# Optimization experiments

Hardware: AMD Instinct MI355X
Metric: run time of the kernel (lower is better)

Reference implementation:

```python
import jax, jax.numpy as jnp
import numpy as np

B, S, D, R, H = 4, 2048, 1024, 256, 8
NI, NP, NO, K = 8, 32, 8, 3
DH = R // H


def _householder_chain(x, vs):
    # x: [B,S,R], vs: [B,S,K,R]; apply K Householder reflections sequentially
    def step(carry, v):
        vn = v * jax.lax.rsqrt(jnp.sum(v * v, axis=-1, keepdims=True) + 1e-8)
        vTx = jnp.sum(carry * vn, axis=-1, keepdims=True)
        return carry - 2.0 * vn * vTx, None
    out, _ = jax.lax.scan(step, x, jnp.moveaxis(vs, 2, 0))
    return out


def _circuit_down(x, in_neurons, proc_neurons, input_weights, proc_idx):
    # soft mixture of input-neuron projections: d_model -> rank
    all_proj = jnp.einsum('bsd,ndr->bsnr', x, in_neurons)
    xr = jnp.einsum('bsnr,bsn->bsr', all_proj, input_weights)
    return _householder_chain(xr, proc_neurons[proc_idx])


def setup_inputs():
    key = jax.random.key(0)
    ks = jax.random.split(key, 14)
    n = lambda k, shape, sc: jax.random.normal(k, shape, jnp.float32) * sc
    inv_d, inv_r = 1.0 / np.sqrt(D), 1.0 / np.sqrt(R)
    return {
        'x': n(ks[0], (B, S, D), 1.0),
        'q_in': n(ks[1], (NI, D, R), inv_d),
        'q_proc': n(ks[2], (NP, R), inv_r),
        'k_in': n(ks[3], (NI, D, R), inv_d),
        'k_proc': n(ks[4], (NP, R), inv_r),
        'v_in': n(ks[5], (NI, D, R), inv_d),
        'v_proc': n(ks[6], (NP, R), inv_r),
        'o_proc': n(ks[7], (NP, R), inv_r),
        'o_out': n(ks[8], (NO, R, D), inv_r),
        'rd_in': n(ks[9], (NI, D), inv_d),
        'rd_proc': n(ks[10], (NP, D), inv_d),
        'ru_out': n(ks[11], (NO, R), inv_r),
        'ru_proc': n(ks[12], (NP, R), inv_r),
    }


def reference(x, q_in, q_proc, k_in, k_proc, v_in, v_proc, o_proc, o_out,
              rd_in, rd_proc, ru_out, ru_proc):
    # --- router (down): soft input weights + top-k process indices ---
    input_weights = jax.nn.softmax(x @ rd_in.T, axis=-1)          # [B,S,NI]
    _, pidx = jax.lax.top_k(x @ rd_proc.T, K)                     # [B,S,K]

    q = _circuit_down(x, q_in, q_proc, input_weights, pidx)      # [B,S,R]
    k = _circuit_down(x, k_in, k_proc, input_weights, pidx)
    v = _circuit_down(x, v_in, v_proc, input_weights, pidx)

    qh = q.reshape(B, S, H, DH)
    kh = k.reshape(B, S, H, DH)
    vh = v.reshape(B, S, H, DH)
    scores = jnp.einsum('bqhd,bkhd->bhqk', qh, kh) / np.sqrt(DH)
    attn = jax.nn.softmax(scores, axis=-1)
    o = jnp.einsum('bhqk,bkhd->bqhd', attn, vh).reshape(B, S, R)  # [B,S,R]

    # --- router (up): soft output weights + top-k process indices ---
    output_weights = jax.nn.softmax(o @ ru_out.T, axis=-1)        # [B,S,NO]
    _, pidx_u = jax.lax.top_k(o @ ru_proc.T, K)                   # [B,S,K]

    oh = _householder_chain(o, o_proc[pidx_u])                    # [B,S,R]
    out = jnp.einsum('bsr,bsn,nrd->bsd', oh, output_weights, o_out)
    return out
```

## Files before the change

### kernel.cpp

```cpp
#include <hip/hip_runtime.h>
#include <math.h>

#define NI 8
#define NP 32
#define TOPK 3

typedef _Float16 f16;
typedef f16 f16x8 __attribute__((ext_vector_type(8)));
typedef f16 f16x4 __attribute__((ext_vector_type(4)));
typedef float f32x4 __attribute__((ext_vector_type(4)));

__device__ __forceinline__ float wave_sum(float v) {
  #pragma unroll
  for (int off = 32; off; off >>= 1) v += __shfl_xor(v, off);
  return v;
}

__device__ __forceinline__ void gload16(const void* g, void* l) {
  __builtin_amdgcn_global_load_lds(
      (const __attribute__((address_space(1))) unsigned int*)g,
      (__attribute__((address_space(3))) unsigned int*)l, 16, 0, 0);
}

__device__ __forceinline__ unsigned int pack_f16x2(float x) {
  f16 h = (f16)x;
  f16 l = (f16)(x - (float)h);
  return (unsigned int)__builtin_bit_cast(unsigned short, h)
       | ((unsigned int)__builtin_bit_cast(unsigned short, l) << 16);
}

__device__ __forceinline__ void unpack8(const unsigned int* p, f16x8& hi, f16x8& lo) {
  uint4 w0 = *reinterpret_cast<const uint4*>(p);
  uint4 w1 = *reinterpret_cast<const uint4*>(p + 4);
  union { unsigned int u[4]; f16x8 v; } H, L;
  H.u[0] = (w0.x & 0xffffu) | (w0.y << 16);
  L.u[0] = (w0.x >> 16)     | (w0.y & 0xffff0000u);
  H.u[1] = (w0.z & 0xffffu) | (w0.w << 16);
  L.u[1] = (w0.z >> 16)     | (w0.w & 0xffff0000u);
  H.u[2] = (w1.x & 0xffffu) | (w1.y << 16);
  L.u[2] = (w1.x >> 16)     | (w1.y & 0xffff0000u);
  H.u[3] = (w1.z & 0xffffu) | (w1.w << 16);
  L.u[3] = (w1.z >> 16)     | (w1.w & 0xffff0000u);
  hi = H.v; lo = L.v;
}

template<int CHUNKS>
__global__ __launch_bounds__(256) void router_kernel(
    const float* __restrict__ X,
    const float* __restrict__ Wsm,
    const float* __restrict__ Wtk,
    float* __restrict__ iw, int* __restrict__ pidx)
{
  const int tid = threadIdx.x, wave = tid >> 6, lane = tid & 63;
  const int t = blockIdx.x * 4 + wave;
  __shared__ float sc[4][40];
  const int Kin = CHUNKS * 256;
  const float4* Xp = reinterpret_cast<const float4*>(X + (size_t)t * Kin);
  float4 xv[CHUNKS];
  #pragma unroll
  for (int c = 0; c < CHUNKS; ++c) xv[c] = Xp[c * 64 + lane];

  for (int w = 0; w < 40; ++w) {
    const float* Wr = (w < NI) ? (Wsm + (size_t)w * Kin) : (Wtk + (size_t)(w - NI) * Kin);
    const float4* Wp = reinterpret_cast<const float4*>(Wr);
    float p = 0.f;
    #pragma unroll
    for (int c = 0; c < CHUNKS; ++c) {
      float4 wv = Wp[c * 64 + lane];
      p = fmaf(xv[c].x, wv.x, p); p = fmaf(xv[c].y, wv.y, p);
      p = fmaf(xv[c].z, wv.z, p); p = fmaf(xv[c].w, wv.w, p);
    }
    p = wave_sum(p);
    if (lane == 0) sc[wave][w] = p;
  }
  float s = (lane < NI) ? sc[wave][lane] : -3.0e38f;
  float m = s;
  #pragma unroll
  for (int off = 4; off; off >>= 1) m = fmaxf(m, __shfl_xor(m, off));
  float e = expf(s - m);
  float sum = e;
  #pragma unroll
  for (int off = 4; off; off >>= 1) sum += __shfl_xor(sum, off);
  if (lane < NI) iw[(size_t)t * NI + lane] = e / sum;

  float v = (lane < NP) ? sc[wave][NI + lane] : -3.0e38f;
  int idx = lane;
  #pragma unroll
  for (int j = 0; j < TOPK; ++j) {
    float bv = v; int bi = idx;
    #pragma unroll
    for (int off = 32; off; off >>= 1) {
      float ov = __shfl_xor(bv, off); int oi = __shfl_xor(bi, off);
      if (ov > bv || (ov == bv && oi < bi)) { bv = ov; bi = oi; }
    }
    if (lane == 0) pidx[t * TOPK + j] = bi;
    if (idx == bi) v = -3.0e38f;
  }
}

__global__ __launch_bounds__(256) void pack_bt(
    const float* __restrict__ S, f16* __restrict__ Dh, f16* __restrict__ Dl,
    int C, int K)
{
  __shared__ float T[64][65];
  const int tid = threadIdx.x;
  const int kb = blockIdx.x * 64, cb = blockIdx.y * 64;
  const int tr = tid >> 4, tc = (tid & 15) * 4;
  #pragma unroll
  for (int i = 0; i < 4; ++i) {
    float4 v = *reinterpret_cast<const float4*>(&S[(size_t)(kb + tr + i * 16) * C + cb + tc]);
    T[tr + i * 16][tc + 0] = v.x; T[tr + i * 16][tc + 1] = v.y;
    T[tr + i * 16][tc + 2] = v.z; T[tr + i * 16][tc + 3] = v.w;
  }
  __syncthreads();
  #pragma unroll
  for (int i = 0; i < 4; ++i) {
    int c = tr + i * 16;
    f16x4 vh, vl;
    #pragma unroll
    for (int q = 0; q < 4; ++q) {
      float a = T[tc + q][c];
      f16 h = (f16)a;
      vh[q] = h;
      vl[q] = (f16)(a - (float)h);
    }
    *reinterpret_cast<f16x4*>(&Dh[(size_t)(cb + c) * K + kb + tc]) = vh;
    *reinterpret_cast<f16x4*>(&Dl[(size_t)(cb + c) * K + kb + tc]) = vl;
  }
}

__global__ __launch_bounds__(256) void pack_split(
    const float* __restrict__ S, f16* __restrict__ Dh, f16* __restrict__ Dl,
    size_t n8)
{
  size_t i = ((size_t)blockIdx.x * 256 + threadIdx.x);
  if (i >= n8) return;
  const float* s = S + i * 8;
  float4 a = *reinterpret_cast<const float4*>(s);
  float4 b = *reinterpret_cast<const float4*>(s + 4);
  float v[8] = {a.x, a.y, a.z, a.w, b.x, b.y, b.z, b.w};
  f16x8 h, l;
  #pragma unroll
  for (int j = 0; j < 8; ++j) {
    f16 hh = (f16)v[j];
    h[j] = hh;
    l[j] = (f16)(v[j] - (float)hh);
  }
  *reinterpret_cast<f16x8*>(Dh + i * 8) = h;
  *reinterpret_cast<f16x8*>(Dl + i * 8) = l;
}

#define TBM 128
#define TBN 128
#define TBK 32

__global__ __launch_bounds__(256, 2) void gemm_split2(
    const f16* __restrict__ Xh, const f16* __restrict__ Xl, int Kin,
    const float* __restrict__ W,
    const f16* __restrict__ Bth, const f16* __restrict__ Btl,
    float* __restrict__ C, int ldC, int Ktot)
{
  __shared__ f16x8 AhL[512];
  __shared__ f16x8 AlL[512];
  __shared__ f16x8 BhL[512];
  __shared__ f16x8 BlL[512];
  __shared__ float Ws[TBM][NI];

  const int tid = threadIdx.x;
  const int wave = tid >> 6, lane = tid & 63;
  const int wm = wave >> 1, wn = wave & 1;
  const int fr = lane & 15, ks = lane >> 4;
  const int row0 = blockIdx.x * TBM, c0 = blockIdx.y * TBN;

  for (int i = tid; i < TBM * NI; i += 256)
    Ws[i >> 3][i & 7] = W[(size_t)(row0 + (i >> 3)) * NI + (i & 7)];

  const int s1 = 256 + tid;
  const int ar0 = tid >> 2, kg0 = ((tid & 3) - (ar0 >> 1)) & 3;
  const int ar1 = s1 >> 2,  kg1 = ((s1 & 3) - (ar1 >> 1)) & 3;

  const f16* xh0 = Xh + (size_t)(row0 + ar0) * Kin + kg0 * 8;
  const f16* xh1 = Xh + (size_t)(row0 + ar1) * Kin + kg1 * 8;
  const f16* xl0 = Xl + (size_t)(row0 + ar0) * Kin + kg0 * 8;
  const f16* xl1 = Xl + (size_t)(row0 + ar1) * Kin + kg1 * 8;
  const f16* bh0 = Bth + (size_t)(c0 + ar0) * Ktot + kg0 * 8;
  const f16* bh1 = Bth + (size_t)(c0 + ar1) * Ktot + kg1 * 8;
  const f16* bl0 = Btl + (size_t)(c0 + ar0) * Ktot + kg0 * 8;
  const f16* bl1 = Btl + (size_t)(c0 + ar1) * Ktot + kg1 * 8;

  f16x8* AhW = &AhL[wave * 64];
  f16x8* AlW = &AlL[wave * 64];
  f16x8* BhW = &BhL[wave * 64];
  f16x8* BlW = &BlL[wave * 64];

  f32x4 acc[4][4] = {};
  f32x4 cac[4][4] = {};

  int n = 0, dk0 = 0;
  for (int kt = 0; kt < Ktot; kt += TBK) {
    __syncthreads();
    gload16(xh0 + dk0, AhW);
    gload16(xh1 + dk0, AhW + 256);
    gload16(xl0 + dk0, AlW);
    gload16(xl1 + dk0, AlW + 256);
    gload16(bh0 + kt, BhW);
    gload16(bh1 + kt, BhW + 256);
    gload16(bl0 + kt, BlW);
    gload16(bl1 + kt, BlW + 256);
    __syncthreads();

    f16x8 ah[4], al[4], bh[4], bl[4];
    #pragma unroll
    for (int mf = 0; mf < 4; ++mf) {
      int ar = wm * 64 + mf * 16 + fr;
      int sl = ar * 4 + (((ar >> 1) + ks) & 3);
      ah[mf] = AhL[sl]; al[mf] = AlL[sl];
    }
    #pragma unroll
    for (int nf = 0; nf < 4; ++nf) {
      int bc = wn * 64 + nf * 16 + fr;
      int sl = bc * 4 + (((bc >> 1) + ks) & 3);
      bh[nf] = BhL[sl]; bl[nf] = BlL[sl];
// ... 17 lines not shown
        float w2 = Ws[wm * 64 + mf * 16 + ks * 4 + 2][n];
        float w3 = Ws[wm * 64 + mf * 16 + ks * 4 + 3][n];
        #pragma unroll
        for (int nf = 0; nf < 4; ++nf) {
          cac[mf][nf][0] = fmaf(w0, acc[mf][nf][0], cac[mf][nf][0]);
          cac[mf][nf][1] = fmaf(w1, acc[mf][nf][1], cac[mf][nf][1]);
          cac[mf][nf][2] = fmaf(w2, acc[mf][nf][2], cac[mf][nf][2]);
          cac[mf][nf][3] = fmaf(w3, acc[mf][nf][3], cac[mf][nf][3]);
          acc[mf][nf] = (f32x4){0.f, 0.f, 0.f, 0.f};
        }
      }
      ++n;
    }
  }

  #pragma unroll
  for (int mf = 0; mf < 4; ++mf)
    #pragma unroll
    for (int nf = 0; nf < 4; ++nf) {
      int col = c0 + wn * 64 + nf * 16 + fr;
      #pragma unroll
      for (int j = 0; j < 4; ++j) {
        int row = row0 + wm * 64 + mf * 16 + ks * 4 + j;
        C[(size_t)row * ldC + col] = cac[mf][nf][j];
      }
    }
}

#define SBM 128
#define SBN 64
#define SBK 32

__global__ __launch_bounds__(256, 3) void gemm_split(
    const float* __restrict__ X, int Kin,
    const float* __restrict__ W,
    const f16* __restrict__ Bth, const f16* __restrict__ Btl,
    float* __restrict__ C, int ldC, int Ktot)
{
  __shared__ f16x8 AhU[SBM * 4];
  __shared__ f16x8 AlU[SBM * 4];
  __shared__ f16x8 BhU[SBN * 4];
  __shared__ f16x8 BlU[SBN * 4];
  __shared__ float Ws[SBM][NI];

  const int tid = threadIdx.x;
  const int row0 = blockIdx.x * SBM;
  const int c0 = blockIdx.y * SBN;

  const int wave = tid >> 6, lane = tid & 63;
  const int wm = wave >> 1, wn = wave & 1;
  const int fr = lane & 15, ks = lane >> 4;

  for (int i = tid; i < SBM * NI; i += 256)
    Ws[i >> 3][i & 7] = W[(size_t)(row0 + (i >> 3)) * NI + (i & 7)];

  const int arow = tid >> 1, ahalf = tid & 1;
  const float* xrow = X + (size_t)(row0 + arow) * Kin + ahalf * 16;
  const int bcol = tid >> 2;
  const int bks = (tid & 3) ^ (bcol & 3);
  const f16* bsh = Bth + (size_t)(c0 + bcol) * Ktot + bks * 8;
  const f16* bsl = Btl + (size_t)(c0 + bcol) * Ktot + bks * 8;

  f32x4 acc[4][2] = {};

  int n = 0, dk0 = 0;
  for (int kt = 0; kt < Ktot; kt += SBK) {
    __syncthreads();
    {
      float4 v0 = *reinterpret_cast<const float4*>(xrow + dk0);
      float4 v1 = *reinterpret_cast<const float4*>(xrow + dk0 + 4);
      float4 v2 = *reinterpret_cast<const float4*>(xrow + dk0 + 8);
      float4 v3 = *reinterpret_cast<const float4*>(xrow + dk0 + 12);
      float wgt = Ws[arow][n];
      float a[16] = {v0.x, v0.y, v0.z, v0.w, v1.x, v1.y, v1.z, v1.w,
                     v2.x, v2.y, v2.z, v2.w, v3.x, v3.y, v3.z, v3.w};
      f16x8 h0, h1, l0, l1;
      #pragma unroll
      for (int j = 0; j < 8; ++j) {
        float p0 = a[j] * wgt, p1 = a[8 + j] * wgt;
        f16 hh0 = (f16)p0, hh1 = (f16)p1;
        h0[j] = hh0; l0[j] = (f16)(p0 - (float)hh0);
        h1[j] = hh1; l1[j] = (f16)(p1 - (float)hh1);
      }
      const int sw = arow & 3;
      AhU[arow * 4 + ((ahalf * 2 + 0) ^ sw)] = h0;
      AhU[arow * 4 + ((ahalf * 2 + 1) ^ sw)] = h1;
      AlU[arow * 4 + ((ahalf * 2 + 0) ^ sw)] = l0;
      AlU[arow * 4 + ((ahalf * 2 + 1) ^ sw)] = l1;
      BhU[tid] = *reinterpret_cast<const f16x8*>(bsh + kt);
      BlU[tid] = *reinterpret_cast<const f16x8*>(bsl + kt);
    }
    __syncthreads();
    f16x8 ah[4], al[4], bh[2], bl[2];
    #pragma unroll
    for (int mf = 0; mf < 4; ++mf) {
      int ar = wm * 64 + mf * 16 + fr;
      int s = ar * 4 + (ks ^ (ar & 3));
      ah[mf] = AhU[s]; al[mf] = AlU[s];
    }
    #pragma unroll
    for (int nf = 0; nf < 2; ++nf) {
      int bc = wn * 32 + nf * 16 + fr;
      int s = bc * 4 + (ks ^ (bc & 3));
      bh[nf] = BhU[s]; bl[nf] = BlU[s];
    }
    #pragma unroll
    for (int mf = 0; mf < 4; ++mf)
      #pragma unroll
      for (int nf = 0; nf < 2; ++nf) {
        acc[mf][nf] = __builtin_amdgcn_mfma_f32_16x16x32_f16(ah[mf], bh[nf], acc[mf][nf], 0, 0, 0);
        acc[mf][nf] = __builtin_amdgcn_mfma_f32_16x16x32_f16(ah[mf], bl[nf], acc[mf][nf], 0, 0, 0);
        acc[mf][nf] = __builtin_amdgcn_mfma_f32_16x16x32_f16(al[mf], bh[nf], acc[mf][nf], 0, 0, 0);
      }
    dk0 += SBK;
    if (dk0 == Kin) { dk0 = 0; ++n; }
  }
  #pragma unroll
  for (int mf = 0; mf < 4; ++mf)
    #pragma unroll
    for (int nf = 0; nf < 2; ++nf) {
      int col = c0 + wn * 32 + nf * 16 + fr;
      #pragma unroll
      for (int j = 0; j < 4; ++j) {
        int row = row0 + wm * 64 + mf * 16 + ks * 4 + j;
        C[(size_t)row * ldC + col] = acc[mf][nf][j];
      }
    }
}

#define GBM 128
#define GBN 128
#define GBK 16
#define GBMp 132

__global__ __launch_bounds__(256) void gemm_mix(
    const float* __restrict__ X, int Kin,
    const float* __restrict__ W,
    const float* __restrict__ Bm0, const float* __restrict__ Bm1, const float* __restrict__ Bm2,
    int ldB, float* __restrict__ C, int ldC, int Nz)
{
  __shared__ float As[GBK][GBMp];
  __shared__ float Bs[GBK][GBMp];
  __shared__ float Ws[GBM][NI];
  const int tid = threadIdx.x;
  const int row0 = blockIdx.x * GBM;
  const int z = blockIdx.z;
  const float* Bm = (z == 0) ? Bm0 : (z == 1) ? Bm1 : Bm2;
  const int c0 = blockIdx.y * GBN;
// ... 40 lines not shown
      #pragma unroll
      for (int i = 0; i < 8; ++i)
        #pragma unroll
        for (int j = 0; j < 8; ++j)
          acc[i][j] = fmaf(av[i], bv[j], acc[i][j]);
    }
    dk0 += GBK;
    if (dk0 == Kin) { dk0 = 0; ++n; }
  }
  #pragma unroll
  for (int i = 0; i < 8; ++i) {
    int row = row0 + tr * 8 + i;
    float* Cp = C + (size_t)row * ldC + z * Nz + c0 + tc * 8;
    float4 o0 = {acc[i][0], acc[i][1], acc[i][2], acc[i][3]};
    float4 o1 = {acc[i][4], acc[i][5], acc[i][6], acc[i][7]};
    *reinterpret_cast<float4*>(Cp) = o0;
    *reinterpret_cast<float4*>(Cp + 4) = o1;
  }
}

__global__ __launch_bounds__(256) void hh_kernel(
    float* __restrict__ X, int ldX,
    const float* __restrict__ P0, const float* __restrict__ P1, const float* __restrict__ P2,
    const int* __restrict__ pidx)
{
  const int tid = threadIdx.x, wave = tid >> 6, lane = tid & 63;
  const int t = blockIdx.x * 4 + wave;
  const int circ = blockIdx.y;
  const float* P = (circ == 0) ? P0 : (circ == 1) ? P1 : P2;
  float* xp = X + (size_t)t * ldX + circ * 256;
  float4 x4 = *reinterpret_cast<float4*>(xp + lane * 4);
  #pragma unroll
  for (int j = 0; j < TOPK; ++j) {
    int id = pidx[t * TOPK + j];
    const float* vp = P + (size_t)id * 256;
    float4 v4 = *reinterpret_cast<const float4*>(vp + lane * 4);
    float ss = v4.x * v4.x + v4.y * v4.y + v4.z * v4.z + v4.w * v4.w;
    ss = wave_sum(ss);
    float inv = 1.0f / sqrtf(ss + 1e-8f);
    float4 vn = {v4.x * inv, v4.y * inv, v4.z * inv, v4.w * inv};
    float dt = vn.x * x4.x + vn.y * x4.y + vn.z * x4.z + vn.w * x4.w;
    dt = wave_sum(dt);
    float d2 = 2.0f * dt;
    x4.x = fmaf(-d2, vn.x, x4.x);
    x4.y = fmaf(-d2, vn.y, x4.y);
    x4.z = fmaf(-d2, vn.z, x4.z);
    x4.w = fmaf(-d2, vn.w, x4.w);
  }
  *reinterpret_cast<float4*>(xp + lane * 4) = x4;
}

__global__ __launch_bounds__(256, 2) void attn_mfma(
    const float* __restrict__ qkv, float* __restrict__ O)
{
  __shared__ f16 Kh[64][40];
  __shared__ f16 Kl[64][40];
  __shared__ unsigned int Vtp[32][68];
  __shared__ unsigned int Pp[4][32][68];

  const int tid = threadIdx.x, wave = tid >> 6, lane = tid & 63;
  const int c = lane & 15, g = lane >> 4;
  const int bh = blockIdx.y, b = bh >> 3, h = bh & 7;
  const int q0 = blockIdx.x * 128;
  const size_t tbase = (size_t)b * 2048;
  const float SCALE = 0.17677669529663687f;

  f16x8 qh[2], ql[2];
  #pragma unroll
  for (int qt = 0; qt < 2; ++qt) {
    const int row = q0 + wave * 32 + qt * 16 + c;
    const float* qp = qkv + (tbase + row) * 768 + h * 32 + g * 8;
    float4 a = *reinterpret_cast<const float4*>(qp);
    float4 b4 = *reinterpret_cast<const float4*>(qp + 4);
    float qv[8] = {a.x, a.y, a.z, a.w, b4.x, b4.y, b4.z, b4.w};
    #pragma unroll
    for (int j = 0; j < 8; ++j) {
      float xs = qv[j] * SCALE;
      f16 hh = (f16)xs;
      qh[qt][j] = hh;
      ql[qt][j] = (f16)(xs - (float)hh);
    }
  }

  f32x4 sacc[2][4];
  f32x4 oacc[2][2] = {};
  float mrow[2][4] = {{-INFINITY, -INFINITY, -INFINITY, -INFINITY},
                      {-INFINITY, -INFINITY, -INFINITY, -INFINITY}};
  float lrow[2][4] = {};

  for (int k0 = 0; k0 < 2048; k0 += 64) {
    __syncthreads();
    {
      const int kj = tid >> 2, dq = (tid & 3) * 8;
      const float* kp = qkv + (tbase + k0 + kj) * 768 + 256 + h * 32 + dq;
      float4 ka = *reinterpret_cast<const float4*>(kp);
      float4 kb = *reinterpret_cast<const float4*>(kp + 4);
      float kv[8] = {ka.x, ka.y, ka.z, ka.w, kb.x, kb.y, kb.z, kb.w};
      f16x8 khi, klo;
      #pragma unroll
      for (int j = 0; j < 8; ++j) {
        f16 hh = (f16)kv[j];
        khi[j] = hh;
        klo[j] = (f16)(kv[j] - (float)hh);
      }
      *reinterpret_cast<f16x8*>(&Kh[kj][dq]) = khi;
      *reinterpret_cast<f16x8*>(&Kl[kj][dq]) = klo;

      const int vk = tid & 63, vq = (tid >> 6) * 8;
      const float* vp = qkv + (tbase + k0 + vk) * 768 + 512 + h * 32 + vq;
      float4 va = *reinterpret_cast<const float4*>(vp);
      float4 vb = *reinterpret_cast<const float4*>(vp + 4);
      float vv[8] = {va.x, va.y, va.z, va.w, vb.x, vb.y, vb.z, vb.w};
      #pragma unroll
      for (int j = 0; j < 8; ++j) Vtp[vq + j][vk] = pack_f16x2(vv[j]);
    }
    __syncthreads();

    #pragma unroll
    for (int s = 0; s < 4; ++s) {
      f16x8 kbh = *reinterpret_cast<const f16x8*>(&Kh[s * 16 + c][g * 8]);
      f16x8 kbl = *reinterpret_cast<const f16x8*>(&Kl[s * 16 + c][g * 8]);
      #pragma unroll
      for (int qt = 0; qt < 2; ++qt) {
        f32x4 acc = {0.f, 0.f, 0.f, 0.f};
        acc = __builtin_amdgcn_mfma_f32_16x16x32_f16(qh[qt], kbh, acc, 0, 0, 0);
        acc = __builtin_amdgcn_mfma_f32_16x16x32_f16(qh[qt], kbl, acc, 0, 0, 0);
        acc = __builtin_amdgcn_mfma_f32_16x16x32_f16(ql[qt], kbh, acc, 0, 0, 0);
        sacc[qt][s] = acc;
      }
    }

    float alpha[2][4];
    #pragma unroll
    for (int qt = 0; qt < 2; ++qt)
      #pragma unroll
      for (int r = 0; r < 4; ++r) {
        float mt = fmaxf(fmaxf(sacc[qt][0][r], sacc[qt][1][r]),
// ... 1 lines not shown
        #pragma unroll
        for (int off = 1; off < 16; off <<= 1) mt = fmaxf(mt, __shfl_xor(mt, off));
        float mn = fmaxf(mrow[qt][r], mt);
        float al = __expf(mrow[qt][r] - mn);
        mrow[qt][r] = mn;
        alpha[qt][r] = al;
        float ps = 0.f;
        #pragma unroll
        for (int s = 0; s < 4; ++s) {
          float p = __expf(sacc[qt][s][r] - mn);
          sacc[qt][s][r] = p;
          ps += p;
        }
        #pragma unroll
        for (int off = 1; off < 16; off <<= 1) ps += __shfl_xor(ps, off);
        lrow[qt][r] = lrow[qt][r] * al + ps;
      }

    #pragma unroll
    for (int qt = 0; qt < 2; ++qt)
      #pragma unroll
      for (int s = 0; s < 4; ++s)
        #pragma unroll
        for (int r = 0; r < 4; ++r)
          Pp[wave][qt * 16 + g * 4 + r][s * 16 + c] = pack_f16x2(sacc[qt][s][r]);

    #pragma unroll
    for (int qt = 0; qt < 2; ++qt)
      #pragma unroll
      for (int dh = 0; dh < 2; ++dh)
        #pragma unroll
        for (int r = 0; r < 4; ++r) oacc[qt][dh][r] *= alpha[qt][r];

    #pragma unroll
    for (int ch = 0; ch < 2; ++ch) {
      f16x8 pah[2], pal[2];
      #pragma unroll
      for (int qt = 0; qt < 2; ++qt)
        unpack8(&Pp[wave][qt * 16 + c][ch * 32 + g * 8], pah[qt], pal[qt]);
      #pragma unroll
      for (int dh = 0; dh < 2; ++dh) {
        f16x8 vh, vl;
        unpack8(&Vtp[dh * 16 + c][ch * 32 + g * 8], vh, vl);
        #pragma unroll
        for (int qt = 0; qt < 2; ++qt) {
          oacc[qt][dh] = __builtin_amdgcn_mfma_f32_16x16x32_f16(pah[qt], vh, oacc[qt][dh], 0, 0, 0);
          oacc[qt][dh] = __builtin_amdgcn_mfma_f32_16x16x32_f16(pah[qt], vl, oacc[qt][dh], 0, 0, 0);
          oacc[qt][dh] = __builtin_amdgcn_mfma_f32_16x16x32_f16(pal[qt], vh, oacc[qt][dh], 0, 0, 0);
        }
      }
    }
  }

  #pragma unroll
  for (int qt = 0; qt < 2; ++qt)
    #pragma unroll
    for (int r = 0; r < 4; ++r) {
      float inv = 1.0f / lrow[qt][r];
      int row = q0 + wave * 32 + qt * 16 + g * 4 + r;
      #pragma unroll
      for (int dh = 0; dh < 2; ++dh)
        O[(tbase + row) * 256 + h * 32 + dh * 16 + c] = oacc[qt][dh][r] * inv;
    }
}

__global__ __launch_bounds__(256) void attn_kernel(
// ... 79 lines not shown
  oacc /= lf;
  O[(tbase + q0 + wave * 2 + r) * 256 + h * 32 + d] = oacc;
}

extern "C" void kernel_launch(void* const* d_in, const int* in_sizes, int n_in,
                              void* d_out, int out_size, void* d_ws, size_t ws_size,
                              hipStream_t stream) {
  const float* x       = (const float*)d_in[0];
  const float* q_in    = (const float*)d_in[1];
  const float* q_proc  = (const float*)d_in[2];
  const float* k_in    = (const float*)d_in[3];
  const float* k_proc  = (const float*)d_in[4];
  const float* v_in    = (const float*)d_in[5];
  const float* v_proc  = (const float*)d_in[6];
  const float* o_proc  = (const float*)d_in[7];
  const float* o_out   = (const float*)d_in[8];
  const float* rd_in   = (const float*)d_in[9];
  const float* rd_proc = (const float*)d_in[10];
  const float* ru_out  = (const float*)d_in[11];
  const float* ru_proc = (const float*)d_in[12];
  float* out = (float*)d_out;
  float* qkv = (float*)d_out;

  const size_t NEED  = (768ull << 10) + 768ull * 8192 * 2 * 2;
  const size_t NEED2 = (768ull << 10) + 768ull * 8192 * 2 * 2
                     + 8192ull * 1024 * 2 * 2;

  if (ws_size >= NEED2) {
    char* wsb = (char*)d_ws;
    float* iw    = (float*)wsb;
    float* owt   = (float*)(wsb + (256 << 10));
    int*   pidx  = (int*)(wsb + (512 << 10));
    int*   pidxu = (int*)(wsb + (640 << 10));
    char*  R1    = wsb + (768 << 10);
    f16* bth_q = (f16*)R1;
    f16* btl_q = (f16*)(R1 + 768ull * 8192 * 2);
    char*  R2    = R1 + 768ull * 8192 * 2 * 2;
    f16* Xh = (f16*)R2;
    f16* Xl = (f16*)(R2 + 8192ull * 1024 * 2);
    float* obuf = (float*)R2;
    f16* Oh    = (f16*)(R2 + (8192ull * 256 * 4));
    f16* Ol    = (f16*)(R2 + (8192ull * 256 * 4) + 8192ull * 256 * 2);
    f16* bth_o = (f16*)(R2 + (8192ull * 256 * 4) + 8192ull * 256 * 2 * 2);
    f16* btl_o = (f16*)(R2 + (8192ull * 256 * 4) + 8192ull * 256 * 2 * 2 + 2048ull * 1024 * 2);

    router_kernel<4><<<dim3(2048), dim3(256), 0, stream>>>(x, rd_in, rd_proc, iw, pidx);
    pack_split<<<dim3(4096), dim3(256), 0, stream>>>(x, Xh, Xl, 8192ull * 1024 / 8);
    pack_bt<<<dim3(128, 4), dim3(256), 0, stream>>>(q_in, bth_q,                 btl_q,                 256, 8192);
    pack_bt<<<dim3(128, 4), dim3(256), 0, stream>>>(k_in, bth_q + 256ull * 8192, btl_q + 256ull * 8192, 256, 8192);
    pack_bt<<<dim3(128, 4), dim3(256), 0, stream>>>(v_in, bth_q + 512ull * 8192, btl_q + 512ull * 8192, 256, 8192);
    gemm_split2<<<dim3(64, 6), dim3(256), 0, stream>>>(Xh, Xl, 1024, iw, bth_q, btl_q, qkv, 768, 8192);
    hh_kernel<<<dim3(2048, 3), dim3(256), 0, stream>>>(qkv, 768, q_proc, k_proc, v_proc, pidx);
    pack_bt<<<dim3(32, 16), dim3(256), 0, stream>>>(o_out, bth_o, btl_o, 1024, 2048);
    attn_mfma<<<dim3(16, 32), dim3(256), 0, stream>>>(qkv, obuf);
    router_kernel<1><<<dim3(2048), dim3(256), 0, stream>>>(obuf, ru_out, ru_proc, owt, pidxu);
    hh_kernel<<<dim3(2048, 1), dim3(256), 0, stream>>>(obuf, 256, o_proc, o_proc, o_proc, pidxu);
    pack_split<<<dim3(1024), dim3(256), 0, stream>>>(obuf, Oh, Ol, 8192ull * 256 / 8);
    gemm_split2<<<dim3(64, 8), dim3(256), 0, stream>>>(Oh, Ol, 256, owt, bth_o, btl_o, out, 1024, 2048);
  } else if (ws_size >= NEED) {
    char* wsb = (char*)d_ws;
    float* iw    = (float*)wsb;
    float* owt   = (float*)(wsb + (256 << 10));
    int*   pidx  = (int*)(wsb + (512 << 10));
    int*   pidxu = (int*)(wsb + (640 << 10));
    char*  Xr    = wsb + (768 << 10);
    f16* bth_q = (f16*)Xr;
    f16* btl_q = (f16*)(Xr + 768ull * 8192 * 2);
    float* obuf = (float*)Xr;
    f16* bth_o = (f16*)(Xr + (8ull << 20));
    f16* btl_o = (f16*)(Xr + (8ull << 20) + 1024ull * 2048 * 2);

    router_kernel<4><<<dim3(2048), dim3(256), 0, stream>>>(x, rd_in, rd_proc, iw, pidx);
    pack_bt<<<dim3(128, 4), dim3(256), 0, stream>>>(q_in, bth_q,                 btl_q,                 256, 8192);
    pack_bt<<<dim3(128, 4), dim3(256), 0, stream>>>(k_in, bth_q + 256ull * 8192, btl_q + 256ull * 8192, 256, 8192);
    pack_bt<<<dim3(128, 4), dim3(256), 0, stream>>>(v_in, bth_q + 512ull * 8192, btl_q + 512ull * 8192, 256, 8192);
    gemm_split<<<dim3(64, 12), dim3(256), 0, stream>>>(x, 1024, iw, bth_q, btl_q, qkv, 768, 8192);
    hh_kernel<<<dim3(2048, 3), dim3(256), 0, stream>>>(qkv, 768, q_proc, k_proc, v_proc, pidx);
    pack_bt<<<dim3(32, 16), dim3(256), 0, stream>>>(o_out, bth_o, btl_o, 1024, 2048);
    attn_mfma<<<dim3(16, 32), dim3(256), 0, stream>>>(qkv, obuf);
    router_kernel<1><<<dim3(2048), dim3(256), 0, stream>>>(obuf, ru_out, ru_proc, owt, pidxu);
    hh_kernel<<<dim3(2048, 1), dim3(256), 0, stream>>>(obuf, 256, o_proc, o_proc, o_proc, pidxu);
    gemm_split<<<dim3(64, 16), dim3(256), 0, stream>>>(obuf, 256, owt, bth_o, btl_o, out, 1024, 2048);
  } else {
    float* ws = (float*)d_ws;
    float* iw    = ws;
    int*   pidx  = (int*)(ws + 65536);
    float* obuf  = ws + 65536 + 24576;
    float* owt   = obuf + 8192 * 256;
    int*   pidxu = (int*)(owt + 65536);

    router_kernel<4><<<dim3(2048), dim3(256), 0, stream>>>(x, rd_in, rd_proc, iw, pidx);
    gemm_mix<<<dim3(64, 2, 3), dim3(256), 0, stream>>>(x, 1024, iw, q_in, k_in, v_in,
                                                       256, qkv, 768, 256);
    hh_kernel<<<dim3(2048, 3), dim3(256), 0, stream>>>(qkv, 768, q_proc, k_proc, v_proc, pidx);
    attn_kernel<<<dim3(256, 32), dim3(256), 0, stream>>>(qkv, obuf);
    router_kernel<1><<<dim3(2048), dim3(256), 0, stream>>>(obuf, ru_out, ru_proc, owt, pidxu);
    hh_kernel<<<dim3(2048, 1), dim3(256), 0, stream>>>(obuf, 256, o_proc, o_proc, o_proc, pidxu);
    gemm_mix<<<dim3(64, 8, 1), dim3(256), 0, stream>>>(obuf, 256, owt, o_out, o_out, o_out,
                                                       1024, out, 1024, 1024);
  }
}
```

Before: 702.3 us.

## Fuse f16 splitting into router and Householder kernels, split-K GEMMs with atomics

The router now handles four tokens per wave and also writes the hi/lo f16 split of x, so the separate pack_split pass goes away. The Householder kernel writes K and V (and the final O) directly as f16 hi/lo pairs, so attention loads pre-split data instead of converting in-kernel, and P and V are stored as separate hi/lo LDS arrays rather than packed words. Both GEMMs are split along the neuron dimension over two z-slices, accumulate with atomicAdd into buffers zeroed by memsets, and raise occupancy to 3 blocks. This adds memset traffic and atomic contention, and the fallback path using gemm_split is removed.

```diff
diff --git a/kernel.cpp b/kernel.cpp
--- a/kernel.cpp
+++ b/kernel.cpp
@@ -22,79 +22,92 @@
       (__attribute__((address_space(3))) unsigned int*)l, 16, 0, 0);
 }
 
-__device__ __forceinline__ unsigned int pack_f16x2(float x) {
-  f16 h = (f16)x;
-  f16 l = (f16)(x - (float)h);
-  return (unsigned int)__builtin_bit_cast(unsigned short, h)
-       | ((unsigned int)__builtin_bit_cast(unsigned short, l) << 16);
-}
-
-__device__ __forceinline__ void unpack8(const unsigned int* p, f16x8& hi, f16x8& lo) {
-  uint4 w0 = *reinterpret_cast<const uint4*>(p);
-  uint4 w1 = *reinterpret_cast<const uint4*>(p + 4);
-  union { unsigned int u[4]; f16x8 v; } H, L;
-  H.u[0] = (w0.x & 0xffffu) | (w0.y << 16);
-  L.u[0] = (w0.x >> 16)     | (w0.y & 0xffff0000u);
-  H.u[1] = (w0.z & 0xffffu) | (w0.w << 16);
-  L.u[1] = (w0.z >> 16)     | (w0.w & 0xffff0000u);
-  H.u[2] = (w1.x & 0xffffu) | (w1.y << 16);
-  L.u[2] = (w1.x >> 16)     | (w1.y & 0xffff0000u);
-  H.u[3] = (w1.z & 0xffffu) | (w1.w << 16);
-  L.u[3] = (w1.z >> 16)     | (w1.w & 0xffff0000u);
-  hi = H.v; lo = L.v;
+__device__ __forceinline__ void split4(float4 v, f16x4& h, f16x4& l) {
+  h[0] = (f16)v.x; l[0] = (f16)(v.x - (float)h[0]);
+  h[1] = (f16)v.y; l[1] = (f16)(v.y - (float)h[1]);
+  h[2] = (f16)v.z; l[2] = (f16)(v.z - (float)h[2]);
+  h[3] = (f16)v.w; l[3] = (f16)(v.w - (float)h[3]);
 }
 
 template<int CHUNKS>
-__global__ __launch_bounds__(256) void router_kernel(
+__global__ __launch_bounds__(256) void router_v2(
     const float* __restrict__ X,
     const float* __restrict__ Wsm,
     const float* __restrict__ Wtk,
-    float* __restrict__ iw, int* __restrict__ pidx)
+    float* __restrict__ iw, int* __restrict__ pidx,
+    f16* __restrict__ Xh, f16* __restrict__ Xl)
 {
+  const int Kin = CHUNKS * 256;
   const int tid = threadIdx.x, wave = tid >> 6, lane = tid & 63;
-  const int t = blockIdx.x * 4 + wave;
-  __shared__ float sc[4][40];
-  const int Kin = CHUNKS * 256;
-  const float4* Xp = reinterpret_cast<const float4*>(X + (size_t)t * Kin);
-  float4 xv[CHUNKS];
-  #pragma unroll
-  for (int c = 0; c < CHUNKS; ++c) xv[c] = Xp[c * 64 + lane];
+  __shared__ float sc[4][4][40];
+  const size_t t0 = (size_t)blockIdx.x * 16 + wave * 4;
+
+  float4 xv[4][CHUNKS];
+  #pragma unroll
+  for (int tt = 0; tt < 4; ++tt) {
+    const float4* Xp = reinterpret_cast<const float4*>(X + (t0 + tt) * Kin);
+    #pragma unroll
+    for (int c = 0; c < CHUNKS; ++c) xv[tt][c] = Xp[c * 64 + lane];
+  }
+  if (Xh) {
+    #pragma unroll
+    for (int tt = 0; tt < 4; ++tt)
+      #pragma unroll
+      for (int c = 0; c < CHUNKS; ++c) {
+        f16x4 h, l;
+        split4(xv[tt][c], h, l);
+        size_t off = (t0 + tt) * Kin + (c * 64 + lane) * 4;
+        *reinterpret_cast<f16x4*>(Xh + off) = h;
+        *reinterpret_cast<f16x4*>(Xl + off) = l;
+      }
+  }
 
   for (int w = 0; w < 40; ++w) {
     const float* Wr = (w < NI) ? (Wsm + (size_t)w * Kin) : (Wtk + (size_t)(w - NI) * Kin);
     const float4* Wp = reinterpret_cast<const float4*>(Wr);
-    float p = 0.f;
+    float p[4] = {};
     #pragma unroll
     for (int c = 0; c < CHUNKS; ++c) {
       float4 wv = Wp[c * 64 + lane];
-      p = fmaf(xv[c].x, wv.x, p); p = fmaf(xv[c].y, wv.y, p);
-      p = fmaf(xv[c].z, wv.z, p); p = fmaf(xv[c].w, wv.w, p);
-    }
-    p = wave_sum(p);
-    if (lane == 0) sc[wave][w] = p;
-  }
-  float s = (lane < NI) ? sc[wave][lane] : -3.0e38f;
-  float m = s;
-  #pragma unroll
-  for (int off = 4; off; off >>= 1) m = fmaxf(m, __shfl_xor(m, off));
-  float e = expf(s - m);
-  float sum = e;
-  #pragma unroll
-  for (int off = 4; off; off >>= 1) sum += __shfl_xor(sum, off);
-  if (lane < NI) iw[(size_t)t * NI + lane] = e / sum;
-
-  float v = (lane < NP) ? sc[wave][NI + lane] : -3.0e38f;
-  int idx = lane;
-  #pragma unroll
-  for (int j = 0; j < TOPK; ++j) {
-    float bv = v; int bi = idx;
-    #pragma unroll
-    for (int off = 32; off; off >>= 1) {
-      float ov = __shfl_xor(bv, off); int oi = __shfl_xor(bi, off);
-      if (ov > bv || (ov == bv && oi < bi)) { bv = ov; bi = oi; }
-    }
-    if (lane == 0) pidx[t * TOPK + j] = bi;
-    if (idx == bi) v = -3.0e38f;
+      #pragma unroll
+      for (int tt = 0; tt < 4; ++tt) {
+        p[tt] = fmaf(xv[tt][c].x, wv.x, p[tt]);
+        p[tt] = fmaf(xv[tt][c].y, wv.y, p[tt]);
+        p[tt] = fmaf(xv[tt][c].z, wv.z, p[tt]);
+        p[tt] = fmaf(xv[tt][c].w, wv.w, p[tt]);
+      }
+    }
+    #pragma unroll
+    for (int tt = 0; tt < 4; ++tt) {
+      p[tt] = wave_sum(p[tt]);
+      if (lane == 0) sc[wave][tt][w] = p[tt];
+    }
+  }
+
+  for (int tt = 0; tt < 4; ++tt) {
+    float s = (lane < NI) ? sc[wave][tt][lane] : -3.0e38f;
+    float m = s;
+    #pragma unroll
+    for (int off = 4; off; off >>= 1) m = fmaxf(m, __shfl_xor(m, off));
+    float e = expf(s - m);
+    float sum = e;
+    #pragma unroll
+    for (int off = 4; off; off >>= 1) sum += __shfl_xor(sum, off);
+    if (lane < NI) iw[(t0 + tt) * NI + lane] = e / sum;
+
+    float v = (lane < NP) ? sc[wave][tt][NI + lane] : -3.0e38f;
+    int idx = lane;
+    #pragma unroll
+    for (int j = 0; j < TOPK; ++j) {
+      float bv = v; int bi = idx;
+      #pragma unroll
+      for (int off = 32; off; off >>= 1) {
+        float ov = __shfl_xor(bv, off); int oi = __shfl_xor(bi, off);
+        if (ov > bv || (ov == bv && oi < bi)) { bv = ov; bi = oi; }
+      }
+      if (lane == 0) pidx[(t0 + tt) * TOPK + j] = bi;
+      if (idx == bi) v = -3.0e38f;
+    }
   }
 }
 
@@ -129,36 +142,15 @@
   }
 }
 
-__global__ __launch_bounds__(256) void pack_split(
-    const float* __restrict__ S, f16* __restrict__ Dh, f16* __restrict__ Dl,
-    size_t n8)
-{
-  size_t i = ((size_t)blockIdx.x * 256 + threadIdx.x);
-  if (i >= n8) return;
-  const float* s = S + i * 8;
-  float4 a = *reinterpret_cast<const float4*>(s);
-  float4 b = *reinterpret_cast<const float4*>(s + 4);
-  float v[8] = {a.x, a.y, a.z, a.w, b.x, b.y, b.z, b.w};
-  f16x8 h, l;
-  #pragma unroll
-  for (int j = 0; j < 8; ++j) {
-    f16 hh = (f16)v[j];
-    h[j] = hh;
-    l[j] = (f16)(v[j] - (float)hh);
-  }
-  *reinterpret_cast<f16x8*>(Dh + i * 8) = h;
-  *reinterpret_cast<f16x8*>(Dl + i * 8) = l;
-}
-
 #define TBM 128
 #define TBN 128
 #define TBK 32
 
-__global__ __launch_bounds__(256, 2) void gemm_split2(
+__global__ __launch_bounds__(256, 3) void gemm_split2(
     const f16* __restrict__ Xh, const f16* __restrict__ Xl, int Kin,
     const float* __restrict__ W,
     const f16* __restrict__ Bth, const f16* __restrict__ Btl,
-    float* __restrict__ C, int ldC, int Ktot)
+    float* __restrict__ C, int ldC, int Ktot, int n_pass)
 {
   __shared__ f16x8 AhL[512];
   __shared__ f16x8 AlL[512];
@@ -171,6 +163,8 @@
   const int wm = wave >> 1, wn = wave & 1;
   const int fr = lane & 15, ks = lane >> 4;
   const int row0 = blockIdx.x * TBM, c0 = blockIdx.y * TBN;
+  const int n_base = blockIdx.z * n_pass;
+  const int koff = n_base * Kin;
 
   for (int i = tid; i < TBM * NI; i += 256)
     Ws[i >> 3][i & 7] = W[(size_t)(row0 + (i >> 3)) * NI + (i & 7)];
@@ -183,10 +177,10 @@
   const f16* xh1 = Xh + (size_t)(row0 + ar1) * Kin + kg1 * 8;
   const f16* xl0 = Xl + (size_t)(row0 + ar0) * Kin + kg0 * 8;
   const f16* xl1 = Xl + (size_t)(row0 + ar1) * Kin + kg1 * 8;
-  const f16* bh0 = Bth + (size_t)(c0 + ar0) * Ktot + kg0 * 8;
-  const f16* bh1 = Bth + (size_t)(c0 + ar1) * Ktot + kg1 * 8;
-  const f16* bl0 = Btl + (size_t)(c0 + ar0) * Ktot + kg0 * 8;
-  const f16* bl1 = Btl + (size_t)(c0 + ar1) * Ktot + kg1 * 8;
+  const f16* bh0 = Bth + (size_t)(c0 + ar0) * Ktot + koff + kg0 * 8;
+  const f16* bh1 = Bth + (size_t)(c0 + ar1) * Ktot + koff + kg1 * 8;
+  const f16* bl0 = Btl + (size_t)(c0 + ar0) * Ktot + koff + kg0 * 8;
+  const f16* bl1 = Btl + (size_t)(c0 + ar1) * Ktot + koff + kg1 * 8;
 
   f16x8* AhW = &AhL[wave * 64];
   f16x8* AlW = &AlL[wave * 64];
@@ -196,8 +190,9 @@
   f32x4 acc[4][4] = {};
   f32x4 cac[4][4] = {};
 
-  int n = 0, dk0 = 0;
-  for (int kt = 0; kt < Ktot; kt += TBK) {
+  int n = n_base, dk0 = 0;
+  const int Kloc = n_pass * Kin;
+  for (int kt = 0; kt < Kloc; kt += TBK) {
     __syncthreads();
     gload16(xh0 + dk0, AhW);
     gload16(xh1 + dk0, AhW + 256);
@@ -261,108 +256,7 @@
       #pragma unroll
       for (int j = 0; j < 4; ++j) {
         int row = row0 + wm * 64 + mf * 16 + ks * 4 + j;
-        C[(size_t)row * ldC + col] = cac[mf][nf][j];
-      }
-    }
-}
-
-#define SBM 128
-#define SBN 64
-#define SBK 32
-
-__global__ __launch_bounds__(256, 3) void gemm_split(
-    const float* __restrict__ X, int Kin,
-    const float* __restrict__ W,
-    const f16* __restrict__ Bth, const f16* __restrict__ Btl,
-    float* __restrict__ C, int ldC, int Ktot)
-{
-  __shared__ f16x8 AhU[SBM * 4];
-  __shared__ f16x8 AlU[SBM * 4];
-  __shared__ f16x8 BhU[SBN * 4];
-  __shared__ f16x8 BlU[SBN * 4];
-  __shared__ float Ws[SBM][NI];
-
-  const int tid = threadIdx.x;
-  const int row0 = blockIdx.x * SBM;
-  const int c0 = blockIdx.y * SBN;
-
-  const int wave = tid >> 6, lane = tid & 63;
-  const int wm = wave >> 1, wn = wave & 1;
-  const int fr = lane & 15, ks = lane >> 4;
-
-  for (int i = tid; i < SBM * NI; i += 256)
-    Ws[i >> 3][i & 7] = W[(size_t)(row0 + (i >> 3)) * NI + (i & 7)];
-
-  const int arow = tid >> 1, ahalf = tid & 1;
-  const float* xrow = X + (size_t)(row0 + arow) * Kin + ahalf * 16;
-  const int bcol = tid >> 2;
-  const int bks = (tid & 3) ^ (bcol & 3);
-  const f16* bsh = Bth + (size_t)(c0 + bcol) * Ktot + bks * 8;
-  const f16* bsl = Btl + (size_t)(c0 + bcol) * Ktot + bks * 8;
-
-  f32x4 acc[4][2] = {};
-
-  int n = 0, dk0 = 0;
-  for (int kt = 0; kt < Ktot; kt += SBK) {
-    __syncthreads();
-    {
-      float4 v0 = *reinterpret_cast<const float4*>(xrow + dk0);
-      float4 v1 = *reinterpret_cast<const float4*>(xrow + dk0 + 4);
-      float4 v2 = *reinterpret_cast<const float4*>(xrow + dk0 + 8);
-      float4 v3 = *reinterpret_cast<const float4*>(xrow + dk0 + 12);
-      float wgt = Ws[arow][n];
-      float a[16] = {v0.x, v0.y, v0.z, v0.w, v1.x, v1.y, v1.z, v1.w,
-                     v2.x, v2.y, v2.z, v2.w, v3.x, v3.y, v3.z, v3.w};
-      f16x8 h0, h1, l0, l1;
-      #pragma unroll
-      for (int j = 0; j < 8; ++j) {
-        float p0 = a[j] * wgt, p1 = a[8 + j] * wgt;
-        f16 hh0 = (f16)p0, hh1 = (f16)p1;
-        h0[j] = hh0; l0[j] = (f16)(p0 - (float)hh0);
-        h1[j] = hh1; l1[j] = (f16)(p1 - (float)hh1);
-      }
-      const int sw = arow & 3;
-      AhU[arow * 4 + ((ahalf * 2 + 0) ^ sw)] = h0;
-      AhU[arow * 4 + ((ahalf * 2 + 1) ^ sw)] = h1;
-      AlU[arow * 4 + ((ahalf * 2 + 0) ^ sw)] = l0;
-      AlU[arow * 4 + ((ahalf * 2 + 1) ^ sw)] = l1;
-      BhU[tid] = *reinterpret_cast<const f16x8*>(bsh + kt);
-      BlU[tid] = *reinterpret_cast<const f16x8*>(bsl + kt);
-    }
-    __syncthreads();
-    f16x8 ah[4], al[4], bh[2], bl[2];
-    #pragma unroll
-    for (int mf = 0; mf < 4; ++mf) {
-      int ar = wm * 64 + mf * 16 + fr;
-      int s = ar * 4 + (ks ^ (ar & 3));
-      ah[mf] = AhU[s]; al[mf] = AlU[s];
-    }
-    #pragma unroll
-    for (int nf = 0; nf < 2; ++nf) {
-      int bc = wn * 32 + nf * 16 + fr;
-      int s = bc * 4 + (ks ^ (bc & 3));
-      bh[nf] = BhU[s]; bl[nf] = BlU[s];
-    }
-    #pragma unroll
-    for (int mf = 0; mf < 4; ++mf)
-      #pragma unroll
-      for (int nf = 0; nf < 2; ++nf) {
-        acc[mf][nf] = __builtin_amdgcn_mfma_f32_16x16x32_f16(ah[mf], bh[nf], acc[mf][nf], 0, 0, 0);
-        acc[mf][nf] = __builtin_amdgcn_mfma_f32_16x16x32_f16(ah[mf], bl[nf], acc[mf][nf], 0, 0, 0);
-        acc[mf][nf] = __builtin_amdgcn_mfma_f32_16x16x32_f16(al[mf], bh[nf], acc[mf][nf], 0, 0, 0);
-      }
-    dk0 += SBK;
-    if (dk0 == Kin) { dk0 = 0; ++n; }
-  }
-  #pragma unroll
-  for (int mf = 0; mf < 4; ++mf)
-    #pragma unroll
-    for (int nf = 0; nf < 2; ++nf) {
-      int col = c0 + wn * 32 + nf * 16 + fr;
-      #pragma unroll
-      for (int j = 0; j < 4; ++j) {
-        int row = row0 + wm * 64 + mf * 16 + ks * 4 + j;
-        C[(size_t)row * ldC + col] = acc[mf][nf][j];
+        atomicAdd(&C[(size_t)row * ldC + col], cac[mf][nf][j]);
       }
     }
 }
@@ -449,7 +343,10 @@
 __global__ __launch_bounds__(256) void hh_kernel(
     float* __restrict__ X, int ldX,
     const float* __restrict__ P0, const float* __restrict__ P1, const float* __restrict__ P2,
-    const int* __restrict__ pidx)
+    const int* __restrict__ pidx,
+    f16* __restrict__ D0h, f16* __restrict__ D0l,
+    f16* __restrict__ D1h, f16* __restrict__ D1l,
+    f16* __restrict__ D2h, f16* __restrict__ D2l)
 {
   const int tid = threadIdx.x, wave = tid >> 6, lane = tid & 63;
   const int t = blockIdx.x * 4 + wave;
@@ -474,16 +371,27 @@
     x4.z = fmaf(-d2, vn.z, x4.z);
     x4.w = fmaf(-d2, vn.w, x4.w);
   }
-  *reinterpret_cast<float4*>(xp + lane * 4) = x4;
-}
-
-__global__ __launch_bounds__(256, 2) void attn_mfma(
-    const float* __restrict__ qkv, float* __restrict__ O)
+  f16* Dh = (circ == 0) ? D0h : (circ == 1) ? D1h : D2h;
+  f16* Dl = (circ == 0) ? D0l : (circ == 1) ? D1l : D2l;
+  if (Dh) {
+    f16x4 h, l;
+    split4(x4, h, l);
+    *reinterpret_cast<f16x4*>(Dh + (size_t)t * 256 + lane * 4) = h;
+    *reinterpret_cast<f16x4*>(Dl + (size_t)t * 256 + lane * 4) = l;
+  } else {
+    *reinterpret_cast<float4*>(xp + lane * 4) = x4;
+  }
+}
+
+__global__ __launch_bounds__(256, 2) void attn_mfma2(
+    const float* __restrict__ qkv,
+    const f16* __restrict__ Khg, const f16* __restrict__ Klg,
+    const f16* __restrict__ Vhg, const f16* __restrict__ Vlg,
+    float* __restrict__ O)
 {
-  __shared__ f16 Kh[64][40];
-  __shared__ f16 Kl[64][40];
-  __shared__ unsigned int Vtp[32][68];
-  __shared__ unsigned int Pp[4][32][68];
+  __shared__ f16 Kh[64][40], Kl[64][40];
+  __shared__ f16 Vh[32][72], Vl[32][72];
+  __shared__ f16 Ph[4][32][72], Pl[4][32][72];
 
   const int tid = threadIdx.x, wave = tid >> 6, lane = tid & 63;
   const int c = lane & 15, g = lane >> 4;
@@ -519,27 +427,16 @@
     __syncthreads();
     {
       const int kj = tid >> 2, dq = (tid & 3) * 8;
-      const float* kp = qkv + (tbase + k0 + kj) * 768 + 256 + h * 32 + dq;
-      float4 ka = *reinterpret_cast<const float4*>(kp);
-      float4 kb = *reinterpret_cast<const float4*>(kp + 4);
-      float kv[8] = {ka.x, ka.y, ka.z, ka.w, kb.x, kb.y, kb.z, kb.w};
-      f16x8 khi, klo;
-      #pragma unroll
-      for (int j = 0; j < 8; ++j) {
-        f16 hh = (f16)kv[j];
-        khi[j] = hh;
-        klo[j] = (f16)(kv[j] - (float)hh);
-      }
-      *reinterpret_cast<f16x8*>(&Kh[kj][dq]) = khi;
-      *reinterpret_cast<f16x8*>(&Kl[kj][dq]) = klo;
+      const size_t krow = (tbase + k0 + kj) * 256 + h * 32 + dq;
+      *reinterpret_cast<f16x8*>(&Kh[kj][dq]) = *reinterpret_cast<const f16x8*>(Khg + krow);
+      *reinterpret_cast<f16x8*>(&Kl[kj][dq]) = *reinterpret_cast<const f16x8*>(Klg + krow);
 
       const int vk = tid & 63, vq = (tid >> 6) * 8;
-      const float* vp = qkv + (tbase + k0 + vk) * 768 + 512 + h * 32 + vq;
-      float4 va = *reinterpret_cast<const float4*>(vp);
-      float4 vb = *reinterpret_cast<const float4*>(vp + 4);
-      float vv[8] = {va.x, va.y, va.z, va.w, vb.x, vb.y, vb.z, vb.w};
-      #pragma unroll
-      for (int j = 0; j < 8; ++j) Vtp[vq + j][vk] = pack_f16x2(vv[j]);
+      const size_t vrow = (tbase + k0 + vk) * 256 + h * 32 + vq;
+      f16x8 vh8 = *reinterpret_cast<const f16x8*>(Vhg + vrow);
+      f16x8 vl8 = *reinterpret_cast<const f16x8*>(Vlg + vrow);
+      #pragma unroll
+      for (int j = 0; j < 8; ++j) { Vh[vq + j][vk] = vh8[j]; Vl[vq + j][vk] = vl8[j]; }
     }
     __syncthreads();
 
@@ -587,8 +484,12 @@
       #pragma unroll
       for (int s = 0; s < 4; ++s)
         #pragma unroll
-        for (int r = 0; r < 4; ++r)
-          Pp[wave][qt * 16 + g * 4 + r][s * 16 + c] = pack_f16x2(sacc[qt][s][r]);
+        for (int r = 0; r < 4; ++r) {
+          float p = sacc[qt][s][r];
+          f16 hh = (f16)p;
+          Ph[wave][qt * 16 + g * 4 + r][s * 16 + c] = hh;
+          Pl[wave][qt * 16 + g * 4 + r][s * 16 + c] = (f16)(p - (float)hh);
+        }
 
     #pragma unroll
     for (int qt = 0; qt < 2; ++qt)
@@ -601,12 +502,14 @@
     for (int ch = 0; ch < 2; ++ch) {
       f16x8 pah[2], pal[2];
       #pragma unroll
-      for (int qt = 0; qt < 2; ++qt)
-        unpack8(&Pp[wave][qt * 16 + c][ch * 32 + g * 8], pah[qt], pal[qt]);
+      for (int qt = 0; qt < 2; ++qt) {
+        pah[qt] = *reinterpret_cast<const f16x8*>(&Ph[wave][qt * 16 + c][ch * 32 + g * 8]);
+        pal[qt] = *reinterpret_cast<const f16x8*>(&Pl[wave][qt * 16 + c][ch * 32 + g * 8]);
+      }
       #pragma unroll
       for (int dh = 0; dh < 2; ++dh) {
-        f16x8 vh, vl;
-        unpack8(&Vtp[dh * 16 + c][ch * 32 + g * 8], vh, vl);
+        f16x8 vh = *reinterpret_cast<const f16x8*>(&Vh[dh * 16 + c][ch * 32 + g * 8]);
+        f16x8 vl = *reinterpret_cast<const f16x8*>(&Vl[dh * 16 + c][ch * 32 + g * 8]);
         #pragma unroll
         for (int qt = 0; qt < 2; ++qt) {
           oacc[qt][dh] = __builtin_amdgcn_mfma_f32_16x16x32_f16(pah[qt], vh, oacc[qt][dh], 0, 0, 0);
@@ -732,9 +635,7 @@
   float* out = (float*)d_out;
   float* qkv = (float*)d_out;
 
-  const size_t NEED  = (768ull << 10) + 768ull * 8192 * 2 * 2;
-  const size_t NEED2 = (768ull << 10) + 768ull * 8192 * 2 * 2
-                     + 8192ull * 1024 * 2 * 2;
+  const size_t NEED2 = (768ull << 10) + 768ull * 8192 * 2 * 2 + 8192ull * 1024 * 2 * 2;
 
   if (ws_size >= NEED2) {
     char* wsb = (char*)d_ws;
@@ -748,49 +649,37 @@
     char*  R2    = R1 + 768ull * 8192 * 2 * 2;
     f16* Xh = (f16*)R2;
     f16* Xl = (f16*)(R2 + 8192ull * 1024 * 2);
-    float* obuf = (float*)R2;
-    f16* Oh    = (f16*)(R2 + (8192ull * 256 * 4));
-    f16* Ol    = (f16*)(R2 + (8192ull * 256 * 4) + 8192ull * 256 * 2);
-    f16* bth_o = (f16*)(R2 + (8192ull * 256 * 4) + 8192ull * 256 * 2 * 2);
-    f16* btl_o = (f16*)(R2 + (8192ull * 256 * 4) + 8192ull * 256 * 2 * 2 + 2048ull * 1024 * 2);
-
-    router_kernel<4><<<dim3(2048), dim3(256), 0, stream>>>(x, rd_in, rd_proc, iw, pidx);
-    pack_split<<<dim3(4096), dim3(256), 0, stream>>>(x, Xh, Xl, 8192ull * 1024 / 8);
+    float* obuf  = (float*)R2;
+    f16* Oh    = (f16*)(R2 + 8388608);
+    f16* Ol    = (f16*)(R2 + 12582912);
+    f16* bth_o = (f16*)(R2 + 16777216);
+    f16* btl_o = (f16*)(R2 + 20971520);
+    f16* Khg   = (f16*)(R2 + 25165824);
+    f16* Klg   = (f16*)(R2 + 29360128);
+    f16* Vhg = (f16*)((char*)d_out + 25165824);
+    f16* Vlg = (f16*)((char*)d_out + 29360128);
+
+    router_v2<4><<<dim3(512), dim3(256), 0, stream>>>(x, rd_in, rd_proc, iw, pidx, Xh, Xl);
     pack_bt<<<dim3(128, 4), dim3(256), 0, stream>>>(q_in, bth_q,                 btl_q,                 256, 8192);
     pack_bt<<<dim3(128, 4), dim3(256), 0, stream>>>(k_in, bth_q + 256ull * 8192, btl_q + 256ull * 8192, 256, 8192);
     pack_bt<<<dim3(128, 4), dim3(256), 0, stream>>>(v_in, bth_q + 512ull * 8192, btl_q + 512ull * 8192, 256, 8192);
-    gemm_split2<<<dim3(64, 6), dim3(256), 0, stream>>>(Xh, Xl, 1024, iw, bth_q, btl_q, qkv, 768, 8192);
-    hh_kernel<<<dim3(2048, 3), dim3(256), 0, stream>>>(qkv, 768, q_proc, k_proc, v_proc, pidx);
+    hipMemsetAsync(qkv, 0, 8192ull * 768 * 4, stream);
+    gemm_split2<<<dim3(64, 6, 2), dim3(256), 0, stream>>>(Xh, Xl, 1024, iw, bth_q, btl_q,
+                                                          qkv, 768, 8192, 4);
+    hh_kernel<<<dim3(2048, 3), dim3(256), 0, stream>>>(qkv, 768, q_proc, k_proc, v_proc, pidx,
+                                                       (f16*)nullptr, (f16*)nullptr,
+                                                       Khg, Klg, Vhg, Vlg);
     pack_bt<<<dim3(32, 16), dim3(256), 0, stream>>>(o_out, bth_o, btl_o, 1024, 2048);
-    attn_mfma<<<dim3(16, 32), dim3(256), 0, stream>>>(qkv, obuf);
-    router_kernel<1><<<dim3(2048), dim3(256), 0, stream>>>(obuf, ru_out, ru_proc, owt, pidxu);
-    hh_kernel<<<dim3(2048, 1), dim3(256), 0, stream>>>(obuf, 256, o_proc, o_proc, o_proc, pidxu);
-    pack_split<<<dim3(1024), dim3(256), 0, stream>>>(obuf, Oh, Ol, 8192ull * 256 / 8);
-    gemm_split2<<<dim3(64, 8), dim3(256), 0, stream>>>(Oh, Ol, 256, owt, bth_o, btl_o, out, 1024, 2048);
-  } else if (ws_size >= NEED) {
-    char* wsb = (char*)d_ws;
-    float* iw    = (float*)wsb;
-    float* owt   = (float*)(wsb + (256 << 10));
-    int*   pidx  = (int*)(wsb + (512 << 10));
-    int*   pidxu = (int*)(wsb + (640 << 10));
-    char*  Xr    = wsb + (768 << 10);
-    f16* bth_q = (f16*)Xr;
-    f16* btl_q = (f16*)(Xr + 768ull * 8192 * 2);
-    float* obuf = (float*)Xr;
-    f16* bth_o = (f16*)(Xr + (8ull << 20));
-    f16* btl_o = (f16*)(Xr + (8ull << 20) + 1024ull * 2048 * 2);
-
-    router_kernel<4><<<dim3(2048), dim3(256), 0, stream>>>(x, rd_in, rd_proc, iw, pidx);
-    pack_bt<<<dim3(128, 4), dim3(256), 0, stream>>>(q_in, bth_q,                 btl_q,                 256, 8192);
-    pack_bt<<<dim3(128, 4), dim3(256), 0, stream>>>(k_in, bth_q + 256ull * 8192, btl_q + 256ull * 8192, 256, 8192);
-    pack_bt<<<dim3(128, 4), dim3(256), 0, stream>>>(v_in, bth_q + 512ull * 8192, btl_q + 512ull * 8192, 256, 8192);
-    gemm_split<<<dim3(64, 12), dim3(256), 0, stream>>>(x, 1024, iw, bth_q, btl_q, qkv, 768, 8192);
-    hh_kernel<<<dim3(2048, 3), dim3(256), 0, stream>>>(qkv, 768, q_proc, k_proc, v_proc, pidx);
-    pack_bt<<<dim3(32, 16), dim3(256), 0, stream>>>(o_out, bth_o, btl_o, 1024, 2048);
-    attn_mfma<<<dim3(16, 32), dim3(256), 0, stream>>>(qkv, obuf);
-    router_kernel<1><<<dim3(2048), dim3(256), 0, stream>>>(obuf, ru_out, ru_proc, owt, pidxu);
-    hh_kernel<<<dim3(2048, 1), dim3(256), 0, stream>>>(obuf, 256, o_proc, o_proc, o_proc, pidxu);
-    gemm_split<<<dim3(64, 16), dim3(256), 0, stream>>>(obuf, 256, owt, bth_o, btl_o, out, 1024, 2048);
+    attn_mfma2<<<dim3(16, 32), dim3(256), 0, stream>>>(qkv, Khg, Klg, Vhg, Vlg, obuf);
+    hipMemsetAsync(d_out, 0, 8192ull * 1024 * 4, stream);
+    router_v2<1><<<dim3(512), dim3(256), 0, stream>>>(obuf, ru_out, ru_proc, owt, pidxu,
+                                                      (f16*)nullptr, (f16*)nullptr);
+    hh_kernel<<<dim3(2048, 1), dim3(256), 0, stream>>>(obuf, 256, o_proc, o_proc, o_proc, pidxu,
+                                                       Oh, Ol,
+                                                       (f16*)nullptr, (f16*)nullptr,
+                                                       (f16*)nullptr, (f16*)nullptr);
+    gemm_split2<<<dim3(64, 8, 2), dim3(256), 0, stream>>>(Oh, Ol, 256, owt, bth_o, btl_o,
+                                                          out, 1024, 2048, 4);
   } else {
     float* ws = (float*)d_ws;
     float* iw    = ws;
@@ -799,13 +688,21 @@
     float* owt   = obuf + 8192 * 256;
     int*   pidxu = (int*)(owt + 65536);
 
-    router_kernel<4><<<dim3(2048), dim3(256), 0, stream>>>(x, rd_in, rd_proc, iw, pidx);
+    router_v2<4><<<dim3(512), dim3(256), 0, stream>>>(x, rd_in, rd_proc, iw, pidx,
+                                                      (f16*)nullptr, (f16*)nullptr);
     gemm_mix<<<dim3(64, 2, 3), dim3(256), 0, stream>>>(x, 1024, iw, q_in, k_in, v_in,
                                                        256, qkv, 768, 256);
-    hh_kernel<<<dim3(2048, 3), dim3(256), 0, stream>>>(qkv, 768, q_proc, k_proc, v_proc, pidx);
+    hh_kernel<<<dim3(2048, 3), dim3(256), 0, stream>>>(qkv, 768, q_proc, k_proc, v_proc, pidx,
+                                                       (f16*)nullptr, (f16*)nullptr,
+                                                       (f16*)nullptr, (f16*)nullptr,
+                                                       (f16*)nullptr, (f16*)nullptr);
     attn_kernel<<<dim3(256, 32), dim3(256), 0, stream>>>(qkv, obuf);
-    router_kernel<1><<<dim3(2048), dim3(256), 0, stream>>>(obuf, ru_out, ru_proc, owt, pidxu);
-    hh_kernel<<<dim3(2048, 1), dim3(256), 0, stream>>>(obuf, 256, o_proc, o_proc, o_proc, pidxu);
+    router_v2<1><<<dim3(512), dim3(256), 0, stream>>>(obuf, ru_out, ru_proc, owt, pidxu,
+                                                      (f16*)nullptr, (f16*)nullptr);
+    hh_kernel<<<dim3(2048, 1), dim3(256), 0, stream>>>(obuf, 256, o_proc, o_proc, o_proc, pidxu,
+                                                       (f16*)nullptr, (f16*)nullptr,
+                                                       (f16*)nullptr, (f16*)nullptr,
+                                                       (f16*)nullptr, (f16*)nullptr);
     gemm_mix<<<dim3(64, 8, 1), dim3(256), 0, stream>>>(obuf, 256, owt, o_out, o_out, o_out,
                                                        1024, out, 1024, 1024);
   }
```

Result: slower. 830.9 us (+18.3%).
